# Performance work log

Measured on AMD Instinct MI355X. Metric: run time of the kernel, lower is better.

## Reference

```python
import jax, jax.numpy as jnp
import numpy as np

HIDDEN = 1024
INTER = 4096
NUM_EXPERTS = 8
TOP_K = 2
LN_EPS = 1e-5


def setup_inputs() -> dict:
    key = jax.random.key(0)
    ks = jax.random.split(key, 8)
    B, S = 4, 2048
    scale = 0.02
    return {
        "hidden_states": jax.random.normal(ks[0], (B, S, HIDDEN), dtype=jnp.float32),
        "ln_scale": jnp.ones((HIDDEN,), jnp.float32),
        "ln_bias": jnp.zeros((HIDDEN,), jnp.float32),
        "router_w": jax.random.normal(ks[1], (NUM_EXPERTS, HIDDEN), jnp.float32) * scale,
        "router_b": jnp.zeros((NUM_EXPERTS,), jnp.float32),
        "up_w": jax.random.normal(ks[2], (NUM_EXPERTS, INTER, HIDDEN), jnp.float32) * scale,
        "up_b": jnp.zeros((NUM_EXPERTS, INTER), jnp.float32),
        "down_w": jax.random.normal(ks[3], (NUM_EXPERTS, HIDDEN, INTER), jnp.float32) * scale,
        "down_b": jnp.zeros((NUM_EXPERTS, HIDDEN), jnp.float32),
    }


def reference(hidden_states, ln_scale, ln_bias, router_w, router_b, up_w, up_b, down_w, down_b):
    B, S, H = hidden_states.shape
    x = hidden_states.reshape(-1, H)  # [T, H]

    # router LayerNorm (eps=1e-5, affine)
    mu = jnp.mean(x, axis=-1, keepdims=True)
    var = jnp.var(x, axis=-1, keepdims=True)
    xn = (x - mu) * jax.lax.rsqrt(var + LN_EPS) * ln_scale + ln_bias

    logits = xn @ router_w.T + router_b                # [T, E]
    top_w, top_idx = jax.lax.top_k(logits, TOP_K)      # [T, K]
    top_w = jax.nn.softmax(top_w.astype(jnp.float32), axis=-1).astype(x.dtype)

    out = jnp.zeros_like(x)
    for e in range(NUM_EXPERTS):
        # per-token combine weight for expert e (0 if not selected)
        gate = jnp.sum(jnp.where(top_idx == e, top_w, 0.0), axis=-1)  # [T]
        # expert MLP (dropout is identity in eval); GELU is exact (erf) as nn.GELU default
        h = jax.nn.gelu(x @ up_w[e].T + up_b[e], approximate=False)
        h = h @ down_w[e].T + down_b[e]
        out = out + gate[:, None] * h
    return out.reshape(B, S, H)
```

## Files before the change

kernel.cpp:

```cpp
#include <hip/hip_runtime.h>
#include <math.h>

#define HIDDEN 1024
#define INTER 4096
#define NE 8

typedef __bf16 bf16;
typedef __bf16 bf16x8 __attribute__((ext_vector_type(8)));
typedef float f32x4 __attribute__((ext_vector_type(4)));

#define WS_CTRL   ((size_t)0)
#define WS_PERM   ((size_t)256)
#define WS_GATES  ((size_t)65792)
#define WS_EIDX   ((size_t)131328)
#define WS_EGATE  ((size_t)196864)
#define WS_XB     ((size_t)262400)
#define WS_UPWB   ((size_t)17039616)
#define WS_DOWNWB ((size_t)84148480)
#define WS_H      ((size_t)151257344)
#define WS_T2S    ((size_t)285475072)
#define WS_Y      WS_UPWB

__device__ __forceinline__ void async_copy16(const void* g, void* l) {
  __builtin_amdgcn_global_load_lds((const __attribute__((address_space(1))) void*)g,
                                   (__attribute__((address_space(3))) void*)l, 16, 0, 0);
}

__device__ __forceinline__ float gelu_erf(float v) {
  float x = v * 0.70710678118654752440f;
  float ax = fabsf(x);
  float t = __builtin_amdgcn_rcpf(fmaf(0.3275911f, ax, 1.0f));
  float p = fmaf(t, 1.061405429f, -1.453152027f);
  p = fmaf(p, t, 1.421413741f);
  p = fmaf(p, t, -0.284496736f);
  p = fmaf(p, t, 0.254829592f);
  p = p * t;
  float e = __expf(-x * x);
  float er = 1.0f - p * e;
  er = copysignf(er, x);
  return 0.5f * v * (1.0f + er);
}

__global__ void cvt_kernel(const float* __restrict__ w, bf16* __restrict__ wb, int n4) {
  int i = blockIdx.x * blockDim.x + threadIdx.x;
  int stride = gridDim.x * blockDim.x;
  for (; i < n4; i += stride) {
    float4 v = ((const float4*)w)[i];
    union { bf16 b[4]; uint2 u; } cv;
    cv.b[0] = (bf16)v.x; cv.b[1] = (bf16)v.y; cv.b[2] = (bf16)v.z; cv.b[3] = (bf16)v.w;
    ((uint2*)wb)[i] = cv.u;
  }
}

__global__ __launch_bounds__(256)
void router_kernel(const float* __restrict__ x, const float* __restrict__ lns,
                   const float* __restrict__ lnb, const float* __restrict__ rw,
                   const float* __restrict__ rb, bf16* __restrict__ xb,
                   int* __restrict__ eidx, float* __restrict__ egate) {
  const int lane = threadIdx.x & 63;
  const int wid = threadIdx.x >> 6;
  const int t = blockIdx.x * 4 + wid;
  const float4* xr = (const float4*)(x + (size_t)t * HIDDEN);
  float4 v[4];
  float s = 0.f, ss = 0.f;
#pragma unroll
  for (int q = 0; q < 4; ++q) {
    v[q] = xr[q * 64 + lane];
    s += v[q].x + v[q].y + v[q].z + v[q].w;
    ss += v[q].x * v[q].x + v[q].y * v[q].y + v[q].z * v[q].z + v[q].w * v[q].w;
  }
#pragma unroll
  for (int o = 32; o; o >>= 1) { s += __shfl_xor(s, o, 64); ss += __shfl_xor(ss, o, 64); }
  const float mu = s * (1.f / HIDDEN);
  const float rstd = rsqrtf(ss * (1.f / HIDDEN) - mu * mu + 1e-5f);
  float acc[NE] = {};
#pragma unroll
  for (int q = 0; q < 4; ++q) {
    int i4 = q * 64 + lane;
    float4 xv = v[q];
    float4 sc = ((const float4*)lns)[i4];
    float4 bi = ((const float4*)lnb)[i4];
    float4 xn;
    xn.x = (xv.x - mu) * rstd * sc.x + bi.x;
    xn.y = (xv.y - mu) * rstd * sc.y + bi.y;
    xn.z = (xv.z - mu) * rstd * sc.z + bi.z;
    xn.w = (xv.w - mu) * rstd * sc.w + bi.w;
#pragma unroll
    for (int e2 = 0; e2 < NE; ++e2) {
      float4 w = ((const float4*)(rw + e2 * HIDDEN))[i4];
      acc[e2] += xn.x * w.x + xn.y * w.y + xn.z * w.z + xn.w * w.w;
    }
    union { bf16 b[4]; uint2 u; } cv;
    cv.b[0] = (bf16)xv.x; cv.b[1] = (bf16)xv.y; cv.b[2] = (bf16)xv.z; cv.b[3] = (bf16)xv.w;
    *(uint2*)&xb[(size_t)t * HIDDEN + i4 * 4] = cv.u;
  }
#pragma unroll
  for (int e2 = 0; e2 < NE; ++e2)
#pragma unroll
    for (int o = 32; o; o >>= 1) acc[e2] += __shfl_xor(acc[e2], o, 64);
  if (lane == 0) {
    float b0 = -1e30f, b1 = -1e30f; int i0 = 0, i1 = 0;
#pragma unroll
    for (int e2 = 0; e2 < NE; ++e2) {
      float lv = acc[e2] + rb[e2];
      if (lv > b0) { b1 = b0; i1 = i0; b0 = lv; i0 = e2; }
      else if (lv > b1) { b1 = lv; i1 = e2; }
    }
    float ex = expf(b1 - b0);
    float g0 = 1.f / (1.f + ex);
    float g1 = ex * g0;
    eidx[t * 2] = i0; eidx[t * 2 + 1] = i1;
    egate[t * 2] = g0; egate[t * 2 + 1] = g1;
  }
}

__global__ __launch_bounds__(256)
void hist_kernel(const int* __restrict__ eidx, int* __restrict__ cnt) {
  __shared__ int h8[NE];
  if (threadIdx.x < NE) h8[threadIdx.x] = 0;
  __syncthreads();
  int i = (blockIdx.x * 256 + threadIdx.x) * 4;
#pragma unroll
  for (int k = 0; k < 4; ++k) atomicAdd(&h8[eidx[i + k]], 1);
  __syncthreads();
  if (threadIdx.x < NE) atomicAdd(&cnt[threadIdx.x], h8[threadIdx.x]);
}

__global__ void scan_kernel(const int* cnt, int* offs) {
  if (threadIdx.x == 0 && blockIdx.x == 0) {
    int a = 0;
    for (int e = 0; e < NE; ++e) { offs[e] = a; a += cnt[e]; }
    offs[NE] = a;
  }
}

__global__ __launch_bounds__(256)
void scatter_kernel(const int* __restrict__ eidx, const float* __restrict__ egate,
                    const int* __restrict__ offs, int* __restrict__ fill,
                    int* __restrict__ perm, float* __restrict__ gates,
                    int* __restrict__ t2s) {
  __shared__ int h8[NE], base8[NE];
  if (threadIdx.x < NE) h8[threadIdx.x] = 0;
  __syncthreads();
  int i = (blockIdx.x * 256 + threadIdx.x) * 4;
  int ee[4], rk[4];
#pragma unroll
  for (int k = 0; k < 4; ++k) { ee[k] = eidx[i + k]; rk[k] = atomicAdd(&h8[ee[k]], 1); }
  __syncthreads();
  if (threadIdx.x < NE) base8[threadIdx.x] = atomicAdd(&fill[threadIdx.x], h8[threadIdx.x]);
  __syncthreads();
#pragma unroll
  for (int k = 0; k < 4; ++k) {
    int entry = i + k;
    int slot = offs[ee[k]] + base8[ee[k]] + rk[k];
    perm[slot] = entry >> 1;
    gates[slot] = egate[entry];
    t2s[entry] = slot;
  }
}

#define READ_A(hh, cb) { \
  _Pragma("unroll") for (int ii = 0; ii < 4; ++ii) \
  _Pragma("unroll") for (int ks = 0; ks < 2; ++ks) { \
    int r_ = wr * 128 + (hh) * 64 + ii * 16 + l15; \
    af[ii][ks] = *(const bf16x8*)&sA[cb][r_ * 64 + (((ks * 4 + l16) ^ (r_ & 7)) * 8)]; \
  } }

#define READ_B(jh, cb) { \
  _Pragma("unroll") for (int jj = 0; jj < 2; ++jj) \
  _Pragma("unroll") for (int ks = 0; ks < 2; ++ks) { \
    int n_ = wc * 64 + ((jh) * 2 + jj) * 16 + l15; \
    bfr[jh][jj][ks] = *(const bf16x8*)&sB[cb][n_ * 64 + (((ks * 4 + l16) ^ (n_ & 7)) * 8)]; \
  } }

#define STAGE_A(ha, nb) { \
  async_copy16(ga[ha][0], &sA[nb][la[ha][0]]); \
  async_copy16(ga[ha][1], &sA[nb][la[ha][1]]); \
  ga[ha][0] += 64; ga[ha][1] += 64; }

#define STAGE_B(hb, nb) { \
  async_copy16(gb[hb][0], &sB[nb][lb[hb][0]]); \
  async_copy16(gb[hb][1], &sB[nb][lb[hb][1]]); \
  gb[hb][0] += 64; gb[hb][1] += 64; }

#define MFMA_CLUSTER(I0, JH) \
  __builtin_amdgcn_s_barrier(); \
  asm volatile("s_waitcnt lgkmcnt(0)" ::: "memory"); \
  __builtin_amdgcn_sched_barrier(0); \
  __builtin_amdgcn_s_setprio(1); \
  { _Pragma("unroll") for (int ii = 0; ii < 4; ++ii) \
    _Pragma("unroll") for (int jj = 0; jj < 2; ++jj) \
    _Pragma("unroll") for (int ks = 0; ks < 2; ++ks) \
      acc[(I0) + ii][(JH) * 2 + jj] = __builtin_amdgcn_mfma_f32_16x16x32_bf16( \
          af[ii][ks], bfr[JH][jj][ks], acc[(I0) + ii][(JH) * 2 + jj], 0, 0, 0); } \
  __builtin_amdgcn_s_setprio(0); \
  __builtin_amdgcn_sched_barrier(0); \
  __builtin_amdgcn_s_barrier();

#define VMW(n) asm volatile("s_waitcnt vmcnt(" #n ")" ::: "memory");

__global__ __launch_bounds__(512, 2)
void up_gemm8(const bf16* __restrict__ xb, const bf16* __restrict__ wb,
              const float* __restrict__ upb, const int* __restrict__ perm,
              const int* __restrict__ offs, bf16* __restrict__ h) {
  const int e = blockIdx.z;
  const int pbase = offs[e];
  const int ne = offs[e + 1] - pbase;
  const int rt = blockIdx.y;
  if (rt * 256 >= ne) return;
  const int ct = blockIdx.x;
  __shared__ __align__(16) bf16 sA[2][256 * 64];
  __shared__ __align__(16) bf16 sB[2][256 * 64];
  const int tid = threadIdx.x;
  const int lane = tid & 63;
  const int wid = tid >> 6;
  const int wr = wid >> 2;
  const int wc = wid & 3;
  const int l15 = lane & 15, l16 = lane >> 4;

  const bf16* ga[2][2]; int la[2][2];
  const bf16* gb[2][2]; int lb[2][2];
  {
    int tr = tid >> 3, tc = tid & 7;
#pragma unroll
    for (int hh = 0; hh < 2; ++hh)
#pragma unroll
      for (int l = 0; l < 2; ++l) {
        int arow = hh * 64 + tr + l * 128;
        int asch = tc ^ (arow & 7);
        int ar = rt * 256 + arow; if (ar > ne - 1) ar = ne - 1;
        int tok = perm[pbase + ar];
        ga[hh][l] = xb + (size_t)tok * HIDDEN + asch * 8;
        la[hh][l] = arow * 64 + tc * 8;
        int rl = l * 64 + tr;
        int brow = hh * 32 + (rl & 31) + (rl >> 5) * 64;
        int bsch = tc ^ (brow & 7);
        int bn = ct * 256 + brow;
        gb[hh][l] = wb + ((size_t)e * INTER + bn) * HIDDEN + bsch * 8;
        lb[hh][l] = brow * 64 + tc * 8;
      }
  }

  f32x4 acc[8][4] = {};
  bf16x8 af[4][2];
  bf16x8 bfr[2][2][2];

  const int NT = HIDDEN / 64;

  STAGE_A(0, 0); STAGE_B(0, 0); STAGE_B(1, 0); STAGE_A(1, 0);
  VMW(4);
  __builtin_amdgcn_s_barrier();

  for (int t = 0; t < NT - 1; ++t) {
    const int cb = t & 1, nb = cb ^ 1;
    READ_A(0, cb); READ_B(0, cb);
    STAGE_A(0, nb);
    VMW(4);
    MFMA_CLUSTER(0, 0);
    READ_B(1, cb);
    STAGE_B(0, nb);
    VMW(4);
    MFMA_CLUSTER(0, 1);
    READ_A(1, cb);
    STAGE_B(1, nb);
    MFMA_CLUSTER(4, 1);
    STAGE_A(1, nb);
    VMW(4);
    MFMA_CLUSTER(4, 0);
  }
  {
    const int cb = (NT - 1) & 1;
    READ_A(0, cb); READ_B(0, cb);
    VMW(0);
    MFMA_CLUSTER(0, 0);
    READ_B(1, cb);
    MFMA_CLUSTER(0, 1);
    READ_A(1, cb);
    MFMA_CLUSTER(4, 1);
    MFMA_CLUSTER(4, 0);
  }

#pragma unroll
  for (int j4 = 0; j4 < 4; ++j4) {
    int c = ct * 256 + wc * 64 + j4 * 16 + l15;
    float bias = upb[e * INTER + c];
#pragma unroll
    for (int i8 = 0; i8 < 8; ++i8) {
#pragma unroll
      for (int tq = 0; tq < 4; ++tq) {
        int r = rt * 256 + wr * 128 + i8 * 16 + l16 * 4 + tq;
        if (r < ne) {
          float v = gelu_erf(acc[i8][j4][tq] + bias);
          h[(size_t)(pbase + r) * INTER + c] = (bf16)v;
        }
      }
    }
  }
}

__global__ __launch_bounds__(256)
void down_gemm(const bf16* __restrict__ h, const bf16* __restrict__ wb,
               const float* __restrict__ dnb, const float* __restrict__ gates,
               const int* __restrict__ offs, float* __restrict__ y) {
  const int e = blockIdx.z;
  const int pbase = offs[e];
  const int ne = offs[e + 1] - pbase;
  const int rt = blockIdx.y;
  if (rt * 128 >= ne) return;
  const int ct = blockIdx.x;
  __shared__ __align__(16) bf16 sA[128 * 64];
  __shared__ __align__(16) bf16 sB[128 * 64];
  const int tid = threadIdx.x;
  const int lane = tid & 63;
  const int wid = tid >> 6;
  const int wr = wid >> 1, wc = wid & 1;
  const int l15 = lane & 15, l16 = lane >> 4;

  const bf16* asrc[4];
  const bf16* bsrc[4];
#pragma unroll
  for (int p = 0; p < 4; ++p) {
    int g = p * 256 + tid;
    int row = g >> 3;
    int sch = (g & 7) ^ (row & 7);
    int ar = rt * 128 + row; if (ar > ne - 1) ar = ne - 1;
    asrc[p] = h + (size_t)(pbase + ar) * INTER + sch * 8;
    int bn = ct * 128 + row;
    bsrc[p] = wb + ((size_t)e * HIDDEN + bn) * INTER + sch * 8;
  }

  f32x4 acc[4][4] = {};

  for (int k0 = 0; k0 < INTER; k0 += 64) {
#pragma unroll
    for (int p = 0; p < 4; ++p)
      async_copy16(asrc[p] + k0, &sA[(size_t)(p * 256 + wid * 64) * 8]);
#pragma unroll
    for (int p = 0; p < 4; ++p)
      async_copy16(bsrc[p] + k0, &sB[(size_t)(p * 256 + wid * 64) * 8]);
    __syncthreads();
#pragma unroll
    for (int ks = 0; ks < 2; ++ks) {
      bf16x8 af[4], bff[4];
#pragma unroll
      for (int i = 0; i < 4; ++i) {
        int r = wr * 64 + i * 16 + l15;
        int ch = (ks * 4 + l16) ^ (r & 7);
        af[i] = *(const bf16x8*)&sA[r * 64 + ch * 8];
      }
#pragma unroll
      for (int j = 0; j < 4; ++j) {
        int n = wc * 64 + j * 16 + l15;
        int ch = (ks * 4 + l16) ^ (n & 7);
        bff[j] = *(const bf16x8*)&sB[n * 64 + ch * 8];
      }
#pragma unroll
      for (int i = 0; i < 4; ++i)
#pragma unroll
        for (int j = 0; j < 4; ++j)
          acc[i][j] = __builtin_amdgcn_mfma_f32_16x16x32_bf16(af[i], bff[j], acc[i][j], 0, 0, 0);
    }
    __syncthreads();
  }

  float bias[4];
#pragma unroll
  for (int j = 0; j < 4; ++j)
    bias[j] = dnb[e * HIDDEN + ct * 128 + wc * 64 + j * 16 + l15];

#pragma unroll
  for (int i = 0; i < 4; ++i) {
#pragma unroll
    for (int t = 0; t < 4; ++t) {
      int r = rt * 128 + wr * 64 + i * 16 + l16 * 4 + t;
      if (r < ne) {
        int slot = pbase + r;
        float gt = gates[slot];
#pragma unroll
        for (int j = 0; j < 4; ++j) {
          int c = ct * 128 + wc * 64 + j * 16 + l15;
          y[(size_t)slot * HIDDEN + c] = gt * (acc[i][j][t] + bias[j]);
        }
      }
    }
  }
}

__global__ __launch_bounds__(256)
void combine_kernel(const float* __restrict__ y, const int* __restrict__ t2s,
                    float* __restrict__ out) {
  int t = blockIdx.x;
  int s0 = t2s[2 * t], s1 = t2s[2 * t + 1];
  const float4* a = (const float4*)(y + (size_t)s0 * HIDDEN);
  const float4* b = (const float4*)(y + (size_t)s1 * HIDDEN);
  float4* o = (float4*)(out + (size_t)t * HIDDEN);
  int c = threadIdx.x;
  float4 va = a[c], vb = b[c];
  o[c] = make_float4(va.x + vb.x, va.y + vb.y, va.z + vb.z, va.w + vb.w);
}

extern "C" void kernel_launch(void* const* d_in, const int* in_sizes, int n_in,
                              void* d_out, int out_size, void* d_ws, size_t ws_size,
                              hipStream_t stream) {
  const float* x   = (const float*)d_in[0];
  const float* lns = (const float*)d_in[1];
  const float* lnb = (const float*)d_in[2];
  const float* rw  = (const float*)d_in[3];
  const float* rb  = (const float*)d_in[4];
  const float* upw = (const float*)d_in[5];
  const float* upb = (const float*)d_in[6];
  const float* dww = (const float*)d_in[7];
  const float* dwb = (const float*)d_in[8];
  float* out = (float*)d_out;

  char* ws = (char*)d_ws;
  int* ctrl   = (int*)(ws + WS_CTRL);
  int* cnt    = ctrl;
  int* fill   = ctrl + 8;
  int* offs   = ctrl + 16;
  int* perm   = (int*)(ws + WS_PERM);
  float* gates = (float*)(ws + WS_GATES);
  int* eidx   = (int*)(ws + WS_EIDX);
  float* egate = (float*)(ws + WS_EGATE);
  bf16* xb    = (bf16*)(ws + WS_XB);
  bf16* upwb  = (bf16*)(ws + WS_UPWB);
  bf16* dwwb  = (bf16*)(ws + WS_DOWNWB);
  bf16* h     = (bf16*)(ws + WS_H);
  int* t2s    = (int*)(ws + WS_T2S);
  float* y    = (float*)(ws + WS_Y);

  const int T = in_sizes[0] / HIDDEN;

  hipMemsetAsync(ctrl, 0, 256, stream);

  cvt_kernel<<<4096, 256, 0, stream>>>(upw, upwb, NE * INTER * HIDDEN / 4);
  cvt_kernel<<<4096, 256, 0, stream>>>(dww, dwwb, NE * HIDDEN * INTER / 4);
  router_kernel<<<T / 4, 256, 0, stream>>>(x, lns, lnb, rw, rb, xb, eidx, egate);
  hist_kernel<<<(2 * T) / 1024, 256, 0, stream>>>(eidx, cnt);
  scan_kernel<<<1, 64, 0, stream>>>(cnt, offs);
  scatter_kernel<<<(2 * T) / 1024, 256, 0, stream>>>(eidx, egate, offs, fill, perm, gates, t2s);

  const int rtiles256 = (T + 255) / 256;
  up_gemm8<<<dim3(INTER / 256, rtiles256, NE), 512, 0, stream>>>(xb, upwb, upb, perm, offs, h);
  const int rtiles = (T + 127) / 128;
  down_gemm<<<dim3(HIDDEN / 128, rtiles, NE), 256, 0, stream>>>(h, dwwb, dwb, gates, offs, y);
  combine_kernel<<<T, 256, 0, stream>>>(y, t2s, out);
}
```

Before: 647.4 us.

## Port down-projection GEMM to the pipelined 256x256 double-buffered 8-wave kernel

Replaces the simple 128x128 single-buffered down GEMM, which synchronises twice per K step, with the same 256x256 tile, 512-thread, double-buffered, interleaved MFMA/stage schedule already used by the up GEMM. The shared main loop is factored into a macro so both kernels use it. This targets load-latency stalls and low data reuse in the down GEMM, the larger of the two GEMMs by K. The cost is far fewer blocks (4 column tiles per expert), which may underfill the GPU's CUs, and a larger shared-memory footprint.

```diff
diff --git a/kernel.cpp b/kernel.cpp
--- a/kernel.cpp
+++ b/kernel.cpp
@@ -198,6 +198,39 @@
   __builtin_amdgcn_s_barrier();
 
 #define VMW(n) asm volatile("s_waitcnt vmcnt(" #n ")" ::: "memory");
+
+#define GEMM8_MAIN_LOOP(NT) \
+  STAGE_A(0, 0); STAGE_B(0, 0); STAGE_B(1, 0); STAGE_A(1, 0); \
+  VMW(4); \
+  __builtin_amdgcn_s_barrier(); \
+  for (int t = 0; t < (NT) - 1; ++t) { \
+    const int cb = t & 1, nb = cb ^ 1; \
+    READ_A(0, cb); READ_B(0, cb); \
+    STAGE_A(0, nb); \
+    VMW(4); \
+    MFMA_CLUSTER(0, 0); \
+    READ_B(1, cb); \
+    STAGE_B(0, nb); \
+    VMW(4); \
+    MFMA_CLUSTER(0, 1); \
+    READ_A(1, cb); \
+    STAGE_B(1, nb); \
+    MFMA_CLUSTER(4, 1); \
+    STAGE_A(1, nb); \
+    VMW(4); \
+    MFMA_CLUSTER(4, 0); \
+  } \
+  { \
+    const int cb = ((NT) - 1) & 1; \
+    READ_A(0, cb); READ_B(0, cb); \
+    VMW(0); \
+    MFMA_CLUSTER(0, 0); \
+    READ_B(1, cb); \
+    MFMA_CLUSTER(0, 1); \
+    READ_A(1, cb); \
+    MFMA_CLUSTER(4, 1); \
+    MFMA_CLUSTER(4, 0); \
+  }
 
 __global__ __launch_bounds__(512, 2)
 void up_gemm8(const bf16* __restrict__ xb, const bf16* __restrict__ wb,
@@ -245,40 +278,7 @@
   bf16x8 af[4][2];
   bf16x8 bfr[2][2][2];
 
-  const int NT = HIDDEN / 64;
-
-  STAGE_A(0, 0); STAGE_B(0, 0); STAGE_B(1, 0); STAGE_A(1, 0);
-  VMW(4);
-  __builtin_amdgcn_s_barrier();
-
-  for (int t = 0; t < NT - 1; ++t) {
-    const int cb = t & 1, nb = cb ^ 1;
-    READ_A(0, cb); READ_B(0, cb);
-    STAGE_A(0, nb);
-    VMW(4);
-    MFMA_CLUSTER(0, 0);
-    READ_B(1, cb);
-    STAGE_B(0, nb);
-    VMW(4);
-    MFMA_CLUSTER(0, 1);
-    READ_A(1, cb);
-    STAGE_B(1, nb);
-    MFMA_CLUSTER(4, 1);
-    STAGE_A(1, nb);
-    VMW(4);
-    MFMA_CLUSTER(4, 0);
-  }
-  {
-    const int cb = (NT - 1) & 1;
-    READ_A(0, cb); READ_B(0, cb);
-    VMW(0);
-    MFMA_CLUSTER(0, 0);
-    READ_B(1, cb);
-    MFMA_CLUSTER(0, 1);
-    READ_A(1, cb);
-    MFMA_CLUSTER(4, 1);
-    MFMA_CLUSTER(4, 0);
-  }
+  GEMM8_MAIN_LOOP(HIDDEN / 64)
 
 #pragma unroll
   for (int j4 = 0; j4 < 4; ++j4) {
@@ -298,88 +298,70 @@
   }
 }
 
-__global__ __launch_bounds__(256)
-void down_gemm(const bf16* __restrict__ h, const bf16* __restrict__ wb,
-               const float* __restrict__ dnb, const float* __restrict__ gates,
-               const int* __restrict__ offs, float* __restrict__ y) {
+__global__ __launch_bounds__(512, 2)
+void down_gemm8(const bf16* __restrict__ hh_, const bf16* __restrict__ wb,
+                const float* __restrict__ dnb, const float* __restrict__ gates,
+                const int* __restrict__ offs, float* __restrict__ y) {
   const int e = blockIdx.z;
   const int pbase = offs[e];
   const int ne = offs[e + 1] - pbase;
   const int rt = blockIdx.y;
-  if (rt * 128 >= ne) return;
+  if (rt * 256 >= ne) return;
   const int ct = blockIdx.x;
-  __shared__ __align__(16) bf16 sA[128 * 64];
-  __shared__ __align__(16) bf16 sB[128 * 64];
+  __shared__ __align__(16) bf16 sA[2][256 * 64];
+  __shared__ __align__(16) bf16 sB[2][256 * 64];
   const int tid = threadIdx.x;
   const int lane = tid & 63;
   const int wid = tid >> 6;
-  const int wr = wid >> 1, wc = wid & 1;
+  const int wr = wid >> 2;
+  const int wc = wid & 3;
   const int l15 = lane & 15, l16 = lane >> 4;
 
-  const bf16* asrc[4];
-  const bf16* bsrc[4];
-#pragma unroll
-  for (int p = 0; p < 4; ++p) {
-    int g = p * 256 + tid;
-    int row = g >> 3;
-    int sch = (g & 7) ^ (row & 7);
-    int ar = rt * 128 + row; if (ar > ne - 1) ar = ne - 1;
-    asrc[p] = h + (size_t)(pbase + ar) * INTER + sch * 8;
-    int bn = ct * 128 + row;
-    bsrc[p] = wb + ((size_t)e * HIDDEN + bn) * INTER + sch * 8;
-  }
-
-  f32x4 acc[4][4] = {};
-
-  for (int k0 = 0; k0 < INTER; k0 += 64) {
-#pragma unroll
-    for (int p = 0; p < 4; ++p)
-      async_copy16(asrc[p] + k0, &sA[(size_t)(p * 256 + wid * 64) * 8]);
-#pragma unroll
-    for (int p = 0; p < 4; ++p)
-      async_copy16(bsrc[p] + k0, &sB[(size_t)(p * 256 + wid * 64) * 8]);
-    __syncthreads();
-#pragma unroll
-    for (int ks = 0; ks < 2; ++ks) {
-      bf16x8 af[4], bff[4];
-#pragma unroll
-      for (int i = 0; i < 4; ++i) {
-        int r = wr * 64 + i * 16 + l15;
-        int ch = (ks * 4 + l16) ^ (r & 7);
-        af[i] = *(const bf16x8*)&sA[r * 64 + ch * 8];
+  const bf16* ga[2][2]; int la[2][2];
+  const bf16* gb[2][2]; int lb[2][2];
+  {
+    int tr = tid >> 3, tc = tid & 7;
+#pragma unroll
+    for (int hhp = 0; hhp < 2; ++hhp)
+#pragma unroll
+      for (int l = 0; l < 2; ++l) {
+        int arow = hhp * 64 + tr + l * 128;
+        int asch = tc ^ (arow & 7);
+        int ar = rt * 256 + arow; if (ar > ne - 1) ar = ne - 1;
+        ga[hhp][l] = hh_ + (size_t)(pbase + ar) * INTER + asch * 8;
+        la[hhp][l] = arow * 64 + tc * 8;
+        int rl = l * 64 + tr;
+        int brow = hhp * 32 + (rl & 31) + (rl >> 5) * 64;
+        int bsch = tc ^ (brow & 7);
+        int bn = ct * 256 + brow;
+        gb[hhp][l] = wb + ((size_t)e * HIDDEN + bn) * INTER + bsch * 8;
+        lb[hhp][l] = brow * 64 + tc * 8;
       }
-#pragma unroll
-      for (int j = 0; j < 4; ++j) {
-        int n = wc * 64 + j * 16 + l15;
-        int ch = (ks * 4 + l16) ^ (n & 7);
-        bff[j] = *(const bf16x8*)&sB[n * 64 + ch * 8];
-      }
-#pragma unroll
-      for (int i = 0; i < 4; ++i)
-#pragma unroll
-        for (int j = 0; j < 4; ++j)
-          acc[i][j] = __builtin_amdgcn_mfma_f32_16x16x32_bf16(af[i], bff[j], acc[i][j], 0, 0, 0);
-    }
-    __syncthreads();
-  }
+  }
+
+  f32x4 acc[8][4] = {};
+  bf16x8 af[4][2];
+  bf16x8 bfr[2][2][2];
+
+  GEMM8_MAIN_LOOP(INTER / 64)
 
   float bias[4];
 #pragma unroll
-  for (int j = 0; j < 4; ++j)
-    bias[j] = dnb[e * HIDDEN + ct * 128 + wc * 64 + j * 16 + l15];
-
-#pragma unroll
-  for (int i = 0; i < 4; ++i) {
-#pragma unroll
-    for (int t = 0; t < 4; ++t) {
-      int r = rt * 128 + wr * 64 + i * 16 + l16 * 4 + t;
+  for (int j4 = 0; j4 < 4; ++j4)
+    bias[j4] = dnb[e * HIDDEN + ct * 256 + wc * 64 + j4 * 16 + l15];
+
+#pragma unroll
+  for (int i8 = 0; i8 < 8; ++i8) {
+#pragma unroll
+    for (int tq = 0; tq < 4; ++tq) {
+      int r = rt * 256 + wr * 128 + i8 * 16 + l16 * 4 + tq;
       if (r < ne) {
         int slot = pbase + r;
         float gt = gates[slot];
 #pragma unroll
-        for (int j = 0; j < 4; ++j) {
-          int c = ct * 128 + wc * 64 + j * 16 + l15;
-          y[(size_t)slot * HIDDEN + c] = gt * (acc[i][j][t] + bias[j]);
+        for (int j4 = 0; j4 < 4; ++j4) {
+          int c = ct * 256 + wc * 64 + j4 * 16 + l15;
+          y[(size_t)slot * HIDDEN + c] = gt * (acc[i8][j4][tq] + bias[j4]);
         }
       }
     }
@@ -442,7 +424,6 @@
 
   const int rtiles256 = (T + 255) / 256;
   up_gemm8<<<dim3(INTER / 256, rtiles256, NE), 512, 0, stream>>>(xb, upwb, upb, perm, offs, h);
-  const int rtiles = (T + 127) / 128;
-  down_gemm<<<dim3(HIDDEN / 128, rtiles, NE), 256, 0, stream>>>(h, dwwb, dwb, gates, offs, y);
+  down_gemm8<<<dim3(HIDDEN / 256, rtiles256, NE), 512, 0, stream>>>(h, dwwb, dwb, gates, offs, y);
   combine_kernel<<<T, 256, 0, stream>>>(y, t2s, out);
 }
```

New measurement: 640.8 us. No clear change (-1.0%).
